# Performance work log

Hardware: AMD Instinct MI355X
Metric: run time of the kernel (lower is better)

The kernel has to match this reference:

```python
import jax, jax.numpy as jnp
import numpy as np

D_MODEL = 1024
NUM_HEADS = 16
DEPTH = D_MODEL // NUM_HEADS
MAX_REL_POS = 128


def setup_inputs() -> dict:
    key = jax.random.key(0)
    ks = jax.random.split(key, 12)
    B, S = 2, 2048
    inp = {
        "q": jax.random.normal(ks[0], (B, S, D_MODEL), jnp.float32),
        "k": jax.random.normal(ks[1], (B, S, D_MODEL), jnp.float32),
        "v": jax.random.normal(ks[2], (B, S, D_MODEL), jnp.float32),
        "mask": jnp.zeros((B, 1, 1, S), jnp.float32),
        "wq": jax.random.normal(ks[3], (D_MODEL, D_MODEL), jnp.float32) * (D_MODEL ** -0.5),
        "bq": jnp.zeros((D_MODEL,), jnp.float32),
        "wk": jax.random.normal(ks[4], (D_MODEL, D_MODEL), jnp.float32) * (D_MODEL ** -0.5),
        "bk": jnp.zeros((D_MODEL,), jnp.float32),
        "wv": jax.random.normal(ks[5], (D_MODEL, D_MODEL), jnp.float32) * (D_MODEL ** -0.5),
        "bv": jnp.zeros((D_MODEL,), jnp.float32),
        "wo": jax.random.normal(ks[6], (D_MODEL, D_MODEL), jnp.float32) * (D_MODEL ** -0.5),
        "bo": jnp.zeros((D_MODEL,), jnp.float32),
        "rel_k_emb": jax.random.normal(ks[7], (2 * MAX_REL_POS + 1, DEPTH), jnp.float32) * 0.02,
        "rel_v_emb": jax.random.normal(ks[8], (2 * MAX_REL_POS + 1, DEPTH), jnp.float32) * 0.02,
    }
    return inp


def _split_heads(x, B):
    # [B, S, d_model] -> [B, H, S, depth]
    S = x.shape[1]
    return x.reshape(B, S, NUM_HEADS, DEPTH).transpose(0, 2, 1, 3)


def reference(q, k, v, mask, wq, bq, wk, bk, wv, bv, wo, bo, rel_k_emb, rel_v_emb):
    B, S, _ = q.shape
    qh = _split_heads(q @ wq + bq, B)  # [B,H,S,d]
    kh = _split_heads(k @ wk + bk, B)
    vh = _split_heads(v @ wv + bv, B)

    # relative position indices [S, S] in [0, 2*MAX_REL_POS]
    ar = jnp.arange(S)
    dist = jnp.clip(ar[None, :] - ar[:, None], -MAX_REL_POS, MAX_REL_POS) + MAX_REL_POS
    rk = rel_k_emb[dist]  # [S, S, depth]
    rv = rel_v_emb[dist]  # [S, S, depth]

    logits = jnp.einsum("bhqd,bhkd->bhqk", qh, kh)
    logits = logits + jnp.einsum("bhqd,qkd->bhqk", qh, rk)
    logits = logits * (1.0 / jnp.sqrt(jnp.float32(DEPTH)))
    logits = logits + mask * -1e9
    attn = jax.nn.softmax(logits, axis=-1)  # [B,H,Sq,Sk]

    out = jnp.einsum("bhqk,bhkd->bhqd", attn, vh)
    out = out + jnp.einsum("bhqk,qkd->bhqd", attn, rv)

    out = out.transpose(0, 2, 1, 3).reshape(B, S, D_MODEL)
    out = out @ wo + bo
    return out, attn
```

## Files before the change

### kernel.cpp

```cpp
#include <hip/hip_runtime.h>
#include <hip/hip_bf16.h>
#include <cstdint>
#include <cstddef>

#define DM   1024
#define NH   16
#define DH   64
#define SEQ  2048
#define BB   2
#define NREL 257
#define BHN  (BB*NH)
#define ROWS (BB*SEQ)

typedef __attribute__((ext_vector_type(8))) short bf16x8;
typedef __attribute__((ext_vector_type(4))) float f32x4;
typedef __attribute__((ext_vector_type(8))) unsigned short us8;

__device__ __forceinline__ unsigned short f2bf(float x){
  union { float f; unsigned u; } v; v.f = x;
  unsigned r = v.u + 0x7fffu + ((v.u >> 16) & 1u);
  return (unsigned short)(r >> 16);
}
__device__ __forceinline__ float b2f(unsigned short h){
  union { unsigned u; float f; } v; v.u = ((unsigned)h) << 16;
  return v.f;
}

__device__ __forceinline__ void gload_lds16(const void* g, void* l){
  __builtin_amdgcn_global_load_lds((const __attribute__((address_space(1))) unsigned int*)g,
                                   (__attribute__((address_space(3))) unsigned int*)l, 16, 0, 0);
}


__global__ void k_split(const float* __restrict__ x, unsigned short* __restrict__ hi,
                        unsigned short* __restrict__ lo, int n){
  int i = blockIdx.x*blockDim.x + threadIdx.x;
  int st = gridDim.x*blockDim.x;
  for (; i < n; i += st){
    float v = x[i];
    unsigned short h = f2bf(v);
    hi[i] = h;
    lo[i] = f2bf(v - b2f(h));
  }
}

__global__ void k_wtrans(const float* __restrict__ W, unsigned short* __restrict__ Thi,
                         unsigned short* __restrict__ Tlo){
  __shared__ float t[64][65];
  int k0 = blockIdx.x*64, n0 = blockIdx.y*64;
  int tid = threadIdx.x;
  for (int u = tid; u < 4096; u += 256){
    int r = u >> 6, c = u & 63;
    t[r][c] = W[(size_t)(k0+r)*DM + n0 + c];
  }
  __syncthreads();
  for (int u = tid; u < 4096; u += 256){
    int r = u >> 6, c = u & 63;
    float v = t[c][r];
    unsigned short h = f2bf(v);
    size_t o = (size_t)(n0+r)*DM + k0 + c;
    Thi[o] = h;
    Tlo[o] = f2bf(v - b2f(h));
  }
}

__global__ void k_embk(const float* __restrict__ e, unsigned short* __restrict__ eb){
  int i = blockIdx.x*256 + threadIdx.x;
  if (i >= 272*64) return;
  int r = i >> 6;
  eb[i] = (r < NREL) ? f2bf(e[i]) : (unsigned short)0;
}

__global__ void k_embt(const float* __restrict__ rv, unsigned short* __restrict__ embT){
  int i = blockIdx.x*256 + threadIdx.x;
  if (i >= 64*256) return;
  int d = i >> 8, j = i & 255;
  embT[i] = (j < 255) ? f2bf(rv[(size_t)(j+1)*DH + d]) : (unsigned short)0;
}

__launch_bounds__(256, 2)
__global__ void k_proj(const unsigned short* __restrict__ Ahi, const unsigned short* __restrict__ Alo,
                       const unsigned short* __restrict__ Bhi, const unsigned short* __restrict__ Blo,
                       const float* __restrict__ bias,
                       unsigned short* __restrict__ Ohi, unsigned short* __restrict__ Olo,
                       int write_lo){
  __shared__ __align__(16) unsigned short sm[4*4096];
  const int tid = threadIdx.x;
  const int w = tid >> 6, lane = tid & 63;
  const int m0 = (blockIdx.x >> 3) * 128;
  const int n0 = (blockIdx.x & 7) * 128;
  const int wr = (w >> 1) * 64, wc = (w & 1) * 64;
  const int fr = lane & 15, fo = (lane >> 4) * 8, fq = (lane >> 4) * 4;

  f32x4 acc[4][4] = {};
  for (int k0 = 0; k0 < DM; k0 += 32){
    const unsigned short* srcs[4] = {
      Ahi + (size_t)m0*DM + k0, Alo + (size_t)m0*DM + k0,
      Bhi + (size_t)n0*DM + k0, Blo + (size_t)n0*DM + k0 };
#pragma unroll
    for (int t = 0; t < 4; ++t)
#pragma unroll
      for (int p = 0; p < 2; ++p){
        int o = p*4096 + tid*16;
        int row = o >> 6, cb = o & 63;
        const char* g = (const char*)(srcs[t] + (size_t)row*DM) + cb;
        char* l = ((char*)sm) + t*8192 + o;
        gload_lds16(g, l);
      }
    __syncthreads();
    bf16x8 a_hi[4], a_lo[4], b_hi[4], b_lo[4];
#pragma unroll
    for (int i = 0; i < 4; ++i){
      int rA = wr + i*16 + fr;
      a_hi[i] = *(const bf16x8*)&sm[0*4096 + rA*32 + fo];
      a_lo[i] = *(const bf16x8*)&sm[1*4096 + rA*32 + fo];
      int rB = wc + i*16 + fr;
      b_hi[i] = *(const bf16x8*)&sm[2*4096 + rB*32 + fo];
      b_lo[i] = *(const bf16x8*)&sm[3*4096 + rB*32 + fo];
    }
#pragma unroll
    for (int i = 0; i < 4; ++i)
#pragma unroll
      for (int j = 0; j < 4; ++j){
        acc[i][j] = __builtin_amdgcn_mfma_f32_16x16x32_bf16(a_hi[i], b_hi[j], acc[i][j], 0,0,0);
        acc[i][j] = __builtin_amdgcn_mfma_f32_16x16x32_bf16(a_hi[i], b_lo[j], acc[i][j], 0,0,0);
        acc[i][j] = __builtin_amdgcn_mfma_f32_16x16x32_bf16(a_lo[i], b_hi[j], acc[i][j], 0,0,0);
      }
    __syncthreads();
  }
#pragma unroll
  for (int i = 0; i < 4; ++i)
#pragma unroll
    for (int j = 0; j < 4; ++j){
      int col = n0 + wc + j*16 + fr;
      float bs = bias[col];
      int h = col >> 6, d = col & 63;
#pragma unroll
      for (int r = 0; r < 4; ++r){
        int row = m0 + wr + i*16 + fq + r;
        int b = row >> 11, s = row & 2047;
        float v = acc[i][j][r] + bs;
        size_t o = ((size_t)(b*NH + h)*SEQ + s)*DH + d;
        unsigned short hh = f2bf(v);
        Ohi[o] = hh;
        if (write_lo) Olo[o] = f2bf(v - b2f(hh));
      }
    }
}

__global__ void k_vtrans(const unsigned short* __restrict__ vh, unsigned short* __restrict__ vt){
  __shared__ __align__(16) unsigned short t[64][72];
  int bh = blockIdx.x >> 5, st = blockIdx.x & 31;
  int s0 = st*64;
  int tid = threadIdx.x;
#pragma unroll
  for (int p = 0; p < 2; ++p){
    int u = tid + p*256;
    int row = u >> 3, ch = u & 7;
    *(us8*)&t[row][ch*8] = *(const us8*)(vh + ((size_t)bh*SEQ + s0 + row)*DH + ch*8);
  }
  __syncthreads();
#pragma unroll
  for (int p = 0; p < 2; ++p){
    int u = tid + p*256;
    int dr = u >> 3, ch = u & 7;
    us8 v;
#pragma unroll
    for (int j = 0; j < 8; ++j) v[j] = t[ch*8+j][dr];
    *(us8*)(vt + ((size_t)bh*DH + dr)*SEQ + s0 + ch*8) = v;
  }
}

__launch_bounds__(256, 2)
__global__ void k_attn(const unsigned short* __restrict__ qhi, const unsigned short* __restrict__ qlo,
                       const unsigned short* __restrict__ khi, const unsigned short* __restrict__ klo,
                       const unsigned short* __restrict__ vt, const unsigned short* __restrict__ embk,
                       const float* __restrict__ mask,
                       unsigned short* __restrict__ Pb, float* __restrict__ Zout,
                       float* __restrict__ ctxu){
  __shared__ unsigned short qrl[64*NREL];
  __shared__ __align__(16) unsigned short Kh[64][72], Kl[64][72], Vt[64][72], Pl[64][72];
  __shared__ float mls[SEQ];

  const int tid = threadIdx.x, w = tid >> 6, lane = tid & 63;
  const int bh = blockIdx.x >> 5, qt = blockIdx.x & 31;
  const int b = bh >> 4;
  const int q0 = qt * 64;
  const int fr = lane & 15, fo = (lane >> 4) * 8, fq = (lane >> 4) * 4;

  for (int i = tid; i < SEQ; i += 256) mls[i] = mask[b*SEQ + i] * (-1e9f);

  bf16x8 q_hi[2], q_lo[2];
  {
    size_t base = ((size_t)bh*SEQ + q0 + w*16 + fr) * DH;
#pragma unroll
    for (int ks = 0; ks < 2; ++ks){
      q_hi[ks] = *(const bf16x8*)(qhi + base + ks*32 + fo);
      q_lo[ks] = *(const bf16x8*)(qlo + base + ks*32 + fo);
    }
  }

#pragma unroll 1
  for (int jt = 0; jt < 17; ++jt){
    f32x4 a = {};
#pragma unroll
    for (int ks = 0; ks < 2; ++ks){
      bf16x8 e = *(const bf16x8*)(embk + ((size_t)(jt*16 + fr))*DH + ks*32 + fo);
      a = __builtin_amdgcn_mfma_f32_16x16x32_bf16(q_hi[ks], e, a, 0,0,0);
    }
    int rr = jt*16 + fr;
#pragma unroll
    for (int r = 0; r < 4; ++r){
      if (rr < NREL) qrl[(w*16 + fq + r)*NREL + rr] = f2bf(a[r]);
    }
  }
  float rcL[4], rcR[4];
#pragma unroll
  for (int r = 0; r < 4; ++r){
    int ql = w*16 + fq + r;
    rcL[r] = b2f(qrl[ql*NREL + 0])   * 0.125f;
    rcR[r] = b2f(qrl[ql*NREL + 256]) * 0.125f;
  }

  const unsigned short* kb_hi = khi + (size_t)bh*SEQ*DH;
  const unsigned short* kb_lo = klo + (size_t)bh*SEQ*DH;
  const unsigned short* vb    = vt  + (size_t)bh*DH*SEQ;

  const int srow = tid >> 3, sch = (tid & 7) * 8;
  us8 rKh[2], rKl[2], rVt[2];
  auto issue = [&](int kt){
#pragma unroll
    for (int p = 0; p < 2; ++p){
      int row = srow + p*32;
      rKh[p] = *(const us8*)(kb_hi + ((size_t)(kt*64 + row))*DH + sch);
      rKl[p] = *(const us8*)(kb_lo + ((size_t)(kt*64 + row))*DH + sch);
      rVt[p] = *(const us8*)(vb + ((size_t)row)*SEQ + kt*64 + sch);
    }
  };
  auto commit = [&](){
#pragma unroll
    for (int p = 0; p < 2; ++p){
      int row = srow + p*32;
      *(us8*)&Kh[row][sch] = rKh[p];
      *(us8*)&Kl[row][sch] = rKl[p];
      *(us8*)&Vt[row][sch] = rVt[p];
    }
  };

  float zpart[4] = {0.f,0.f,0.f,0.f};
  f32x4 ctx[4] = {};

  issue(0); commit();
  __syncthreads();

#pragma unroll 1
  for (int kt = 0; kt < 32; ++kt){
    if (kt < 31) issue(kt + 1);

    const bool leftU  = (kt*64 + 191) <= q0;
    const bool rightU = (kt*64) >= (q0 + 191);

    float pv[4][4];
#pragma unroll
    for (int c = 0; c < 4; ++c){
      f32x4 a = {};
#pragma unroll
      for (int ks = 0; ks < 2; ++ks){
        bf16x8 kf = *(const bf16x8*)&Kh[c*16 + fr][ks*32 + fo];
        bf16x8 lf = *(const bf16x8*)&Kl[c*16 + fr][ks*32 + fo];
        a = __builtin_amdgcn_mfma_f32_16x16x32_bf16(q_hi[ks], kf, a, 0,0,0);
        a = __builtin_amdgcn_mfma_f32_16x16x32_bf16(q_hi[ks], lf, a, 0,0,0);
        a = __builtin_amdgcn_mfma_f32_16x16x32_bf16(q_lo[ks], kf, a, 0,0,0);
      }
      int kg = kt*64 + c*16 + fr;
      float mv = mls[kg];
      if (leftU){
#pragma unroll
        for (int r = 0; r < 4; ++r)
          pv[c][r] = __expf(a[r]*0.125f + rcL[r] + mv);
      } else if (rightU){
#pragma unroll
        for (int r = 0; r < 4; ++r)
          pv[c][r] = __expf(a[r]*0.125f + rcR[r] + mv);
      } else {
#pragma unroll
        for (int r = 0; r < 4; ++r){
          int ql = w*16 + fq + r;
          int qg = q0 + ql;
          int dd = kg - qg; dd = min(max(dd, -128), 128);
          float rel = b2f(qrl[ql*NREL + dd + 128]);
          pv[c][r] = __expf((a[r] + rel)*0.125f + mv);
        }
      }
    }
#pragma unroll
    for (int r = 0; r < 4; ++r)
      zpart[r] += pv[0][r] + pv[1][r] + pv[2][r] + pv[3][r];
#pragma unroll
    for (int c = 0; c < 4; ++c)
#pragma unroll
      for (int r = 0; r < 4; ++r)
        Pl[w*16 + fq + r][c*16 + fr] = f2bf(pv[c][r]);
    {
      int lr = lane >> 2, ch = lane & 3;
      const unsigned short* src = &Pl[w*16 + lr][0];
      size_t gbase = ((size_t)bh*SEQ + q0 + w*16 + lr)*SEQ + kt*64;
      *(us8*)(Pb + gbase + ch*8)     = *(const us8*)(src + ch*8);
      *(us8*)(Pb + gbase + (ch+4)*8) = *(const us8*)(src + (ch+4)*8);
    }
#pragma unroll
    for (int ks = 0; ks < 2; ++ks){
      bf16x8 pf = *(const bf16x8*)&Pl[w*16 + fr][ks*32 + fo];
#pragma unroll
      for (int j = 0; j < 4; ++j){
        bf16x8 vf = *(const bf16x8*)&Vt[j*16 + fr][ks*32 + fo];
        ctx[j] = __builtin_amdgcn_mfma_f32_16x16x32_bf16(pf, vf, ctx[j], 0,0,0);
      }
    }
    if (kt < 31){
      __syncthreads();
      commit();
      __syncthreads();
    }
  }

#pragma unroll
  for (int r = 0; r < 4; ++r){
    float part = zpart[r];
    part += __shfl_xor(part, 1);
    part += __shfl_xor(part, 2);
    part += __shfl_xor(part, 4);
    part += __shfl_xor(part, 8);
    zpart[r] = part;
  }
  if (fr == 0){
#pragma unroll
    for (int r = 0; r < 4; ++r)
      Zout[(size_t)bh*SEQ + q0 + w*16 + fq + r] = zpart[r];
  }
#pragma unroll
  for (int j = 0; j < 4; ++j)
#pragma unroll
    for (int r = 0; r < 4; ++r)
      ctxu[((size_t)bh*SEQ + q0 + w*16 + fq + r)*DH + j*16 + fr] = ctx[j][r];
}

__launch_bounds__(256, 4)
__global__ void k_norm(const unsigned short* __restrict__ Pb, float* __restrict__ attn,
                       const float* __restrict__ Z,
                       const float* __restrict__ ctxu, const unsigned short* __restrict__ embT,
                       const float* __restrict__ rv, unsigned short* __restrict__ ctxb){
  __shared__ __align__(16) unsigned short band[64*256];
  __shared__ float invr[64], Lr[64], Rr[64];
  const int tid = threadIdx.x, w = tid >> 6, lane = tid & 63;
  const int bh = blockIdx.x >> 5, qt = blockIdx.x & 31;
  const int q0 = qt * 64;
  const int fr = lane & 15, fo = (lane >> 4) * 8, fq = (lane >> 4) * 4;

  {
    us8 z = {0,0,0,0,0,0,0,0};
    for (int i = tid; i < 64*256/8; i += 256) ((us8*)band)[i] = z;
  }
  __syncthreads();

#pragma unroll 1
  for (int rr = 0; rr < 16; ++rr){
    int rl = w*16 + rr;
    int q = q0 + rl;
    size_t R = (size_t)bh*SEQ + q;
    float inv = 1.0f / Z[R];
    float la = 0.f, ra = 0.f;
    const us8* prow = (const us8*)(Pb + R*SEQ);
    float4* orow = (float4*)(attn + R*SEQ);
    unsigned short* brow = band + rl*256;
    const int sw = (rl & 7) << 3;
#pragma unroll 1
    for (int c = 0; c < 4; ++c){
      us8 p8 = prow[c*64 + lane];
      float pe[8];
#pragma unroll
      for (int e = 0; e < 8; ++e) pe[e] = b2f(p8[e]);
      float4 o0 = {pe[0]*inv, pe[1]*inv, pe[2]*inv, pe[3]*inv};
      float4 o1 = {pe[4]*inv, pe[5]*inv, pe[6]*inv, pe[7]*inv};
      orow[(c*64 + lane)*2]     = o0;
      orow[(c*64 + lane)*2 + 1] = o1;
      int jlo = c*512 - q + 127;
      if (jlo + 511 < 0){
        la += pe[0]+pe[1]+pe[2]+pe[3]+pe[4]+pe[5]+pe[6]+pe[7];
      } else if (jlo > 254){
        ra += pe[0]+pe[1]+pe[2]+pe[3]+pe[4]+pe[5]+pe[6]+pe[7];
      } else {
        int jb = jlo + lane*8;
#pragma unroll
        for (int e = 0; e < 8; ++e){
          int j = jb + e;
          if (j < 0)        la += pe[e];
          else if (j > 254) ra += pe[e];
          else              brow[j ^ sw] = p8[e];
        }
      }
    }
#pragma unroll
    for (int m = 1; m < 64; m <<= 1){
      la += __shfl_xor(la, m);
      ra += __shfl_xor(ra, m);
    }
    if (lane == 0){ invr[rl] = inv; Lr[rl] = la; Rr[rl] = ra; }
  }
  __syncthreads();

  f32x4 acc[4] = {};
  {
    const int arow = w*16 + fr;
    const int asw = (arow & 7) << 3;
    const unsigned short* bandr = band + arow*256;
#pragma unroll
    for (int kk = 0; kk < 8; ++kk){
      bf16x8 af = *(const bf16x8*)&bandr[(kk*32 + fo) ^ asw];
#pragma unroll
      for (int jt = 0; jt < 4; ++jt){
        bf16x8 bfr = *(const bf16x8*)(embT + (size_t)(jt*16 + fr)*256 + kk*32 + fo);
        acc[jt] = __builtin_amdgcn_mfma_f32_16x16x32_bf16(af, bfr, acc[jt], 0,0,0);
      }
    }
  }

  const int b = bh >> 4, h = bh & 15;
#pragma unroll
  for (int jt = 0; jt < 4; ++jt){
    int d = jt*16 + fr;
    float e0 = rv[d], e256 = rv[(size_t)256*DH + d];
#pragma unroll
    for (int r = 0; r < 4; ++r){
      int rl = w*16 + fq + r;
      int q = q0 + rl;
      float cv = (ctxu[((size_t)bh*SEQ + q)*DH + d] + acc[jt][r] + Lr[rl]*e0 + Rr[rl]*e256) * invr[rl];
      ctxb[((size_t)b*SEQ + q)*DM + h*DH + d] = f2bf(cv);
    }
  }
}

__launch_bounds__(256, 2)
__global__ void k_out(const unsigned short* __restrict__ A, const unsigned short* __restrict__ Bt,
                      const float* __restrict__ bias, float* __restrict__ out){
  __shared__ __align__(16) unsigned short sm[2*4096];
  const int tid = threadIdx.x;
  const int w = tid >> 6, lane = tid & 63;
  const int m0 = (blockIdx.x >> 3) * 128;
  const int n0 = (blockIdx.x & 7) * 128;
  const int wr = (w >> 1) * 64, wc = (w & 1) * 64;
  const int fr = lane & 15, fo = (lane >> 4)*8, fq = (lane >> 4)*4;
  f32x4 acc[4][4] = {};
  for (int k0 = 0; k0 < DM; k0 += 32){
    const unsigned short* srcs[2] = { A + (size_t)m0*DM + k0, Bt + (size_t)n0*DM + k0 };
#pragma unroll
    for (int t = 0; t < 2; ++t)
#pragma unroll
      for (int p = 0; p < 2; ++p){
        int o = p*4096 + tid*16;
        int row = o >> 6, cb = o & 63;
        const char* g = (const char*)(srcs[t] + (size_t)row*DM) + cb;
        char* l = ((char*)sm) + t*8192 + o;
        gload_lds16(g, l);
      }
    __syncthreads();
    bf16x8 af[4], bf[4];
#pragma unroll
    for (int i = 0; i < 4; ++i){
      af[i] = *(const bf16x8*)&sm[0*4096 + (wr + i*16 + fr)*32 + fo];
      bf[i] = *(const bf16x8*)&sm[1*4096 + (wc + i*16 + fr)*32 + fo];
    }
#pragma unroll
    for (int i = 0; i < 4; ++i)
#pragma unroll
      for (int j = 0; j < 4; ++j)
        acc[i][j] = __builtin_amdgcn_mfma_f32_16x16x32_bf16(af[i], bf[j], acc[i][j], 0,0,0);
    __syncthreads();
  }
#pragma unroll
  for (int i = 0; i < 4; ++i)
#pragma unroll
    for (int j = 0; j < 4; ++j){
      int col = n0 + wc + j*16 + fr;
      float bs = bias[col];
#pragma unroll
      for (int r = 0; r < 4; ++r){
        int row = m0 + wr + i*16 + fq + r;
        out[(size_t)row*DM + col] = acc[i][j][r] + bs;
      }
    }
}

extern "C" void kernel_launch(void* const* d_in, const int* in_sizes, int n_in,
                              void* d_out, int out_size, void* d_ws, size_t ws_size,
                              hipStream_t stream){
  const float* q    = (const float*)d_in[0];
  const float* k    = (const float*)d_in[1];
  const float* v    = (const float*)d_in[2];
  const float* mask = (const float*)d_in[3];
  const float* wq   = (const float*)d_in[4];
  const float* bq   = (const float*)d_in[5];
  const float* wk   = (const float*)d_in[6];
  const float* bk   = (const float*)d_in[7];
  const float* wv   = (const float*)d_in[8];
  const float* bv   = (const float*)d_in[9];
  const float* wo   = (const float*)d_in[10];
  const float* bo   = (const float*)d_in[11];
  const float* rk   = (const float*)d_in[12];
  const float* rv   = (const float*)d_in[13];

  float* out  = (float*)d_out;
  float* attn = out + (size_t)ROWS*DM;

  char* p = (char*)d_ws;
  size_t used = 0;
  auto alloc = [&](size_t bytes) -> char* {
    char* r = p;
    size_t a = (bytes + 255) & ~(size_t)255;
    p += a; used += a;
    return r;
  };
  const size_t NE  = (size_t)ROWS*DM;
  unsigned short* q_hi = (unsigned short*)alloc(NE*2);
  unsigned short* q_lo = (unsigned short*)alloc(NE*2);
  unsigned short* k_hi = (unsigned short*)alloc(NE*2);
  unsigned short* k_lo = (unsigned short*)alloc(NE*2);
  unsigned short* v_hi = (unsigned short*)alloc(NE*2);
  unsigned short* v_lo = (unsigned short*)alloc(NE*2);
  unsigned short* wqt_hi = (unsigned short*)alloc((size_t)DM*DM*2);
  unsigned short* wqt_lo = (unsigned short*)alloc((size_t)DM*DM*2);
  unsigned short* wkt_hi = (unsigned short*)alloc((size_t)DM*DM*2);
  unsigned short* wkt_lo = (unsigned short*)alloc((size_t)DM*DM*2);
  unsigned short* wvt_hi = (unsigned short*)alloc((size_t)DM*DM*2);
  unsigned short* wvt_lo = (unsigned short*)alloc((size_t)DM*DM*2);
  unsigned short* wot_hi = (unsigned short*)alloc((size_t)DM*DM*2);
  unsigned short* wot_lo = (unsigned short*)alloc((size_t)DM*DM*2);
  unsigned short* qh_hi = (unsigned short*)alloc(NE*2);
  unsigned short* qh_lo = (unsigned short*)alloc(NE*2);
  unsigned short* kh_hi = (unsigned short*)alloc(NE*2);
  unsigned short* kh_lo = (unsigned short*)alloc(NE*2);
  unsigned short* vh    = (unsigned short*)alloc(NE*2);
  unsigned short* vht   = (unsigned short*)alloc(NE*2);
  unsigned short* embk  = (unsigned short*)alloc((size_t)272*64*2);
  unsigned short* embT  = (unsigned short*)alloc((size_t)64*256*2);
  float* Zb   = (float*)alloc((size_t)BHN*SEQ*4);
  float* ctxu = (float*)alloc((size_t)BHN*SEQ*DH*4);
  unsigned short* ctxb = (unsigned short*)alloc(NE*2);
  unsigned short* Pb   = (unsigned short*)alloc((size_t)BHN*SEQ*SEQ*2);
  if (used > ws_size) return;

  int n = (int)NE;
  k_split<<<2048, 256, 0, stream>>>(q, q_hi, q_lo, n);
  k_split<<<2048, 256, 0, stream>>>(k, k_hi, k_lo, n);
  k_split<<<2048, 256, 0, stream>>>(v, v_hi, v_lo, n);
  dim3 tg(16,16);
  k_wtrans<<<tg, 256, 0, stream>>>(wq, wqt_hi, wqt_lo);
  k_wtrans<<<tg, 256, 0, stream>>>(wk, wkt_hi, wkt_lo);
  k_wtrans<<<tg, 256, 0, stream>>>(wv, wvt_hi, wvt_lo);
  k_wtrans<<<tg, 256, 0, stream>>>(wo, wot_hi, wot_lo);
  k_embk<<<(272*64+255)/256, 256, 0, stream>>>(rk, embk);
  k_embt<<<64, 256, 0, stream>>>(rv, embT);

  k_proj<<<256, 256, 0, stream>>>(q_hi, q_lo, wqt_hi, wqt_lo, bq, qh_hi, qh_lo, 1);
  k_proj<<<256, 256, 0, stream>>>(k_hi, k_lo, wkt_hi, wkt_lo, bk, kh_hi, kh_lo, 1);
  k_proj<<<256, 256, 0, stream>>>(v_hi, v_lo, wvt_hi, wvt_lo, bv, vh, vh, 0);
  k_vtrans<<<1024, 256, 0, stream>>>(vh, vht);

  k_attn<<<1024, 256, 0, stream>>>(qh_hi, qh_lo, kh_hi, kh_lo, vht, embk, mask, Pb, Zb, ctxu);
  k_norm<<<1024, 256, 0, stream>>>(Pb, attn, Zb, ctxu, embT, rv, ctxb);
  k_out<<<256, 256, 0, stream>>>(ctxb, wot_hi, bo, out);
}
```

Measured before the change: 625.8 us.

## Drop split-bf16 compensation and use plain bf16 for projections and QK logits

Removes the hi/lo bf16 split emulation of fp32 throughout: inputs and weights are cast once to single bf16, projections use one MFMA per tile instead of three, and the QK^T logits in attention use a single bf16 product. This cuts MFMA work, LDS traffic and workspace memory traffic for the split buffers, and the input cast is vectorized to float4. The trade is reduced accuracy in the logits and projections, which may push results toward the tolerance limit. It also clamps the embedding load indices so padded entries no longer read out of bounds.

```diff
diff --git a/kernel.cpp b/kernel.cpp
--- a/kernel.cpp
+++ b/kernel.cpp
@@ -15,6 +15,7 @@
 typedef __attribute__((ext_vector_type(8))) short bf16x8;
 typedef __attribute__((ext_vector_type(4))) float f32x4;
 typedef __attribute__((ext_vector_type(8))) unsigned short us8;
+typedef __attribute__((ext_vector_type(4))) unsigned short us4;
 
 __device__ __forceinline__ unsigned short f2bf(float x){
   union { float f; unsigned u; } v; v.f = x;
@@ -32,20 +33,17 @@
 }
 
 
-__global__ void k_split(const float* __restrict__ x, unsigned short* __restrict__ hi,
-                        unsigned short* __restrict__ lo, int n){
+__global__ void k_cast(const float* __restrict__ x, unsigned short* __restrict__ o, int n4){
   int i = blockIdx.x*blockDim.x + threadIdx.x;
   int st = gridDim.x*blockDim.x;
-  for (; i < n; i += st){
-    float v = x[i];
-    unsigned short h = f2bf(v);
-    hi[i] = h;
-    lo[i] = f2bf(v - b2f(h));
-  }
-}
-
-__global__ void k_wtrans(const float* __restrict__ W, unsigned short* __restrict__ Thi,
-                         unsigned short* __restrict__ Tlo){
+  for (; i < n4; i += st){
+    float4 f = ((const float4*)x)[i];
+    us4 v = { f2bf(f.x), f2bf(f.y), f2bf(f.z), f2bf(f.w) };
+    *(us4*)(o + (size_t)i*4) = v;
+  }
+}
+
+__global__ void k_wtrans(const float* __restrict__ W, unsigned short* __restrict__ T){
   __shared__ float t[64][65];
   int k0 = blockIdx.x*64, n0 = blockIdx.y*64;
   int tid = threadIdx.x;
@@ -56,11 +54,7 @@
   __syncthreads();
   for (int u = tid; u < 4096; u += 256){
     int r = u >> 6, c = u & 63;
-    float v = t[c][r];
-    unsigned short h = f2bf(v);
-    size_t o = (size_t)(n0+r)*DM + k0 + c;
-    Thi[o] = h;
-    Tlo[o] = f2bf(v - b2f(h));
+    T[(size_t)(n0+r)*DM + k0 + c] = f2bf(t[c][r]);
   }
 }
 
@@ -68,37 +62,33 @@
   int i = blockIdx.x*256 + threadIdx.x;
   if (i >= 272*64) return;
   int r = i >> 6;
-  eb[i] = (r < NREL) ? f2bf(e[i]) : (unsigned short)0;
+  float v = e[min(i, NREL*64 - 1)];
+  eb[i] = (r < NREL) ? f2bf(v) : (unsigned short)0;
 }
 
 __global__ void k_embt(const float* __restrict__ rv, unsigned short* __restrict__ embT){
   int i = blockIdx.x*256 + threadIdx.x;
   if (i >= 64*256) return;
   int d = i >> 8, j = i & 255;
-  embT[i] = (j < 255) ? f2bf(rv[(size_t)(j+1)*DH + d]) : (unsigned short)0;
+  float v = rv[(size_t)min(j+1, 256)*DH + d];
+  embT[i] = (j < 255) ? f2bf(v) : (unsigned short)0;
 }
 
 __launch_bounds__(256, 2)
-__global__ void k_proj(const unsigned short* __restrict__ Ahi, const unsigned short* __restrict__ Alo,
-                       const unsigned short* __restrict__ Bhi, const unsigned short* __restrict__ Blo,
-                       const float* __restrict__ bias,
-                       unsigned short* __restrict__ Ohi, unsigned short* __restrict__ Olo,
-                       int write_lo){
-  __shared__ __align__(16) unsigned short sm[4*4096];
+__global__ void k_proj(const unsigned short* __restrict__ A, const unsigned short* __restrict__ Bt,
+                       const float* __restrict__ bias, unsigned short* __restrict__ O){
+  __shared__ __align__(16) unsigned short sm[2*4096];
   const int tid = threadIdx.x;
   const int w = tid >> 6, lane = tid & 63;
   const int m0 = (blockIdx.x >> 3) * 128;
   const int n0 = (blockIdx.x & 7) * 128;
   const int wr = (w >> 1) * 64, wc = (w & 1) * 64;
-  const int fr = lane & 15, fo = (lane >> 4) * 8, fq = (lane >> 4) * 4;
-
+  const int fr = lane & 15, fo = (lane >> 4)*8, fq = (lane >> 4)*4;
   f32x4 acc[4][4] = {};
   for (int k0 = 0; k0 < DM; k0 += 32){
-    const unsigned short* srcs[4] = {
-      Ahi + (size_t)m0*DM + k0, Alo + (size_t)m0*DM + k0,
-      Bhi + (size_t)n0*DM + k0, Blo + (size_t)n0*DM + k0 };
-#pragma unroll
-    for (int t = 0; t < 4; ++t)
+    const unsigned short* srcs[2] = { A + (size_t)m0*DM + k0, Bt + (size_t)n0*DM + k0 };
+#pragma unroll
+    for (int t = 0; t < 2; ++t)
 #pragma unroll
       for (int p = 0; p < 2; ++p){
         int o = p*4096 + tid*16;
@@ -108,24 +98,17 @@
         gload_lds16(g, l);
       }
     __syncthreads();
-    bf16x8 a_hi[4], a_lo[4], b_hi[4], b_lo[4];
+    bf16x8 af[4], bf[4];
 #pragma unroll
     for (int i = 0; i < 4; ++i){
-      int rA = wr + i*16 + fr;
-      a_hi[i] = *(const bf16x8*)&sm[0*4096 + rA*32 + fo];
-      a_lo[i] = *(const bf16x8*)&sm[1*4096 + rA*32 + fo];
-      int rB = wc + i*16 + fr;
-      b_hi[i] = *(const bf16x8*)&sm[2*4096 + rB*32 + fo];
-      b_lo[i] = *(const bf16x8*)&sm[3*4096 + rB*32 + fo];
+      af[i] = *(const bf16x8*)&sm[0*4096 + (wr + i*16 + fr)*32 + fo];
+      bf[i] = *(const bf16x8*)&sm[1*4096 + (wc + i*16 + fr)*32 + fo];
     }
 #pragma unroll
     for (int i = 0; i < 4; ++i)
 #pragma unroll
-      for (int j = 0; j < 4; ++j){
-        acc[i][j] = __builtin_amdgcn_mfma_f32_16x16x32_bf16(a_hi[i], b_hi[j], acc[i][j], 0,0,0);
-        acc[i][j] = __builtin_amdgcn_mfma_f32_16x16x32_bf16(a_hi[i], b_lo[j], acc[i][j], 0,0,0);
-        acc[i][j] = __builtin_amdgcn_mfma_f32_16x16x32_bf16(a_lo[i], b_hi[j], acc[i][j], 0,0,0);
-      }
+      for (int j = 0; j < 4; ++j)
+        acc[i][j] = __builtin_amdgcn_mfma_f32_16x16x32_bf16(af[i], bf[j], acc[i][j], 0,0,0);
     __syncthreads();
   }
 #pragma unroll
@@ -139,11 +122,7 @@
       for (int r = 0; r < 4; ++r){
         int row = m0 + wr + i*16 + fq + r;
         int b = row >> 11, s = row & 2047;
-        float v = acc[i][j][r] + bs;
-        size_t o = ((size_t)(b*NH + h)*SEQ + s)*DH + d;
-        unsigned short hh = f2bf(v);
-        Ohi[o] = hh;
-        if (write_lo) Olo[o] = f2bf(v - b2f(hh));
+        O[((size_t)(b*NH + h)*SEQ + s)*DH + d] = f2bf(acc[i][j][r] + bs);
       }
     }
 }
@@ -172,14 +151,13 @@
 }
 
 __launch_bounds__(256, 2)
-__global__ void k_attn(const unsigned short* __restrict__ qhi, const unsigned short* __restrict__ qlo,
-                       const unsigned short* __restrict__ khi, const unsigned short* __restrict__ klo,
+__global__ void k_attn(const unsigned short* __restrict__ qh, const unsigned short* __restrict__ kh,
                        const unsigned short* __restrict__ vt, const unsigned short* __restrict__ embk,
                        const float* __restrict__ mask,
                        unsigned short* __restrict__ Pb, float* __restrict__ Zout,
                        float* __restrict__ ctxu){
   __shared__ unsigned short qrl[64*NREL];
-  __shared__ __align__(16) unsigned short Kh[64][72], Kl[64][72], Vt[64][72], Pl[64][72];
+  __shared__ __align__(16) unsigned short Kh[64][72], Vt[64][72], Pl[64][72];
   __shared__ float mls[SEQ];
 
   const int tid = threadIdx.x, w = tid >> 6, lane = tid & 63;
@@ -190,14 +168,12 @@
 
   for (int i = tid; i < SEQ; i += 256) mls[i] = mask[b*SEQ + i] * (-1e9f);
 
-  bf16x8 q_hi[2], q_lo[2];
+  bf16x8 q_hi[2];
   {
     size_t base = ((size_t)bh*SEQ + q0 + w*16 + fr) * DH;
 #pragma unroll
-    for (int ks = 0; ks < 2; ++ks){
-      q_hi[ks] = *(const bf16x8*)(qhi + base + ks*32 + fo);
-      q_lo[ks] = *(const bf16x8*)(qlo + base + ks*32 + fo);
-    }
+    for (int ks = 0; ks < 2; ++ks)
+      q_hi[ks] = *(const bf16x8*)(qh + base + ks*32 + fo);
   }
 
 #pragma unroll 1
@@ -222,18 +198,16 @@
     rcR[r] = b2f(qrl[ql*NREL + 256]) * 0.125f;
   }
 
-  const unsigned short* kb_hi = khi + (size_t)bh*SEQ*DH;
-  const unsigned short* kb_lo = klo + (size_t)bh*SEQ*DH;
-  const unsigned short* vb    = vt  + (size_t)bh*DH*SEQ;
+  const unsigned short* kb = kh + (size_t)bh*SEQ*DH;
+  const unsigned short* vb = vt + (size_t)bh*DH*SEQ;
 
   const int srow = tid >> 3, sch = (tid & 7) * 8;
-  us8 rKh[2], rKl[2], rVt[2];
+  us8 rKh[2], rVt[2];
   auto issue = [&](int kt){
 #pragma unroll
     for (int p = 0; p < 2; ++p){
       int row = srow + p*32;
-      rKh[p] = *(const us8*)(kb_hi + ((size_t)(kt*64 + row))*DH + sch);
-      rKl[p] = *(const us8*)(kb_lo + ((size_t)(kt*64 + row))*DH + sch);
+      rKh[p] = *(const us8*)(kb + ((size_t)(kt*64 + row))*DH + sch);
       rVt[p] = *(const us8*)(vb + ((size_t)row)*SEQ + kt*64 + sch);
     }
   };
@@ -242,7 +216,6 @@
     for (int p = 0; p < 2; ++p){
       int row = srow + p*32;
       *(us8*)&Kh[row][sch] = rKh[p];
-      *(us8*)&Kl[row][sch] = rKl[p];
       *(us8*)&Vt[row][sch] = rVt[p];
     }
   };
@@ -267,10 +240,7 @@
 #pragma unroll
       for (int ks = 0; ks < 2; ++ks){
         bf16x8 kf = *(const bf16x8*)&Kh[c*16 + fr][ks*32 + fo];
-        bf16x8 lf = *(const bf16x8*)&Kl[c*16 + fr][ks*32 + fo];
         a = __builtin_amdgcn_mfma_f32_16x16x32_bf16(q_hi[ks], kf, a, 0,0,0);
-        a = __builtin_amdgcn_mfma_f32_16x16x32_bf16(q_hi[ks], lf, a, 0,0,0);
-        a = __builtin_amdgcn_mfma_f32_16x16x32_bf16(q_lo[ks], kf, a, 0,0,0);
       }
       int kg = kt*64 + c*16 + fr;
       float mv = mls[kg];
@@ -521,52 +491,43 @@
     return r;
   };
   const size_t NE  = (size_t)ROWS*DM;
-  unsigned short* q_hi = (unsigned short*)alloc(NE*2);
-  unsigned short* q_lo = (unsigned short*)alloc(NE*2);
-  unsigned short* k_hi = (unsigned short*)alloc(NE*2);
-  unsigned short* k_lo = (unsigned short*)alloc(NE*2);
-  unsigned short* v_hi = (unsigned short*)alloc(NE*2);
-  unsigned short* v_lo = (unsigned short*)alloc(NE*2);
-  unsigned short* wqt_hi = (unsigned short*)alloc((size_t)DM*DM*2);
-  unsigned short* wqt_lo = (unsigned short*)alloc((size_t)DM*DM*2);
-  unsigned short* wkt_hi = (unsigned short*)alloc((size_t)DM*DM*2);
-  unsigned short* wkt_lo = (unsigned short*)alloc((size_t)DM*DM*2);
-  unsigned short* wvt_hi = (unsigned short*)alloc((size_t)DM*DM*2);
-  unsigned short* wvt_lo = (unsigned short*)alloc((size_t)DM*DM*2);
-  unsigned short* wot_hi = (unsigned short*)alloc((size_t)DM*DM*2);
-  unsigned short* wot_lo = (unsigned short*)alloc((size_t)DM*DM*2);
-  unsigned short* qh_hi = (unsigned short*)alloc(NE*2);
-  unsigned short* qh_lo = (unsigned short*)alloc(NE*2);
-  unsigned short* kh_hi = (unsigned short*)alloc(NE*2);
-  unsigned short* kh_lo = (unsigned short*)alloc(NE*2);
-  unsigned short* vh    = (unsigned short*)alloc(NE*2);
-  unsigned short* vht   = (unsigned short*)alloc(NE*2);
-  unsigned short* embk  = (unsigned short*)alloc((size_t)272*64*2);
-  unsigned short* embT  = (unsigned short*)alloc((size_t)64*256*2);
+  unsigned short* qb   = (unsigned short*)alloc(NE*2);
+  unsigned short* kbf  = (unsigned short*)alloc(NE*2);
+  unsigned short* vbf  = (unsigned short*)alloc(NE*2);
+  unsigned short* wqt  = (unsigned short*)alloc((size_t)DM*DM*2);
+  unsigned short* wkt  = (unsigned short*)alloc((size_t)DM*DM*2);
+  unsigned short* wvt  = (unsigned short*)alloc((size_t)DM*DM*2);
+  unsigned short* wot  = (unsigned short*)alloc((size_t)DM*DM*2);
+  unsigned short* qh   = (unsigned short*)alloc(NE*2);
+  unsigned short* kh   = (unsigned short*)alloc(NE*2);
+  unsigned short* vh   = (unsigned short*)alloc(NE*2);
+  unsigned short* vht  = (unsigned short*)alloc(NE*2);
+  unsigned short* embk = (unsigned short*)alloc((size_t)272*64*2);
+  unsigned short* embT = (unsigned short*)alloc((size_t)64*256*2);
   float* Zb   = (float*)alloc((size_t)BHN*SEQ*4);
   float* ctxu = (float*)alloc((size_t)BHN*SEQ*DH*4);
   unsigned short* ctxb = (unsigned short*)alloc(NE*2);
   unsigned short* Pb   = (unsigned short*)alloc((size_t)BHN*SEQ*SEQ*2);
   if (used > ws_size) return;
 
-  int n = (int)NE;
-  k_split<<<2048, 256, 0, stream>>>(q, q_hi, q_lo, n);
-  k_split<<<2048, 256, 0, stream>>>(k, k_hi, k_lo, n);
-  k_split<<<2048, 256, 0, stream>>>(v, v_hi, v_lo, n);
+  const int N4 = (int)(NE/4);
+  k_cast<<<2048, 256, 0, stream>>>(q, qb, N4);
+  k_cast<<<2048, 256, 0, stream>>>(k, kbf, N4);
+  k_cast<<<2048, 256, 0, stream>>>(v, vbf, N4);
   dim3 tg(16,16);
-  k_wtrans<<<tg, 256, 0, stream>>>(wq, wqt_hi, wqt_lo);
-  k_wtrans<<<tg, 256, 0, stream>>>(wk, wkt_hi, wkt_lo);
-  k_wtrans<<<tg, 256, 0, stream>>>(wv, wvt_hi, wvt_lo);
-  k_wtrans<<<tg, 256, 0, stream>>>(wo, wot_hi, wot_lo);
+  k_wtrans<<<tg, 256, 0, stream>>>(wq, wqt);
+  k_wtrans<<<tg, 256, 0, stream>>>(wk, wkt);
+  k_wtrans<<<tg, 256, 0, stream>>>(wv, wvt);
+  k_wtrans<<<tg, 256, 0, stream>>>(wo, wot);
   k_embk<<<(272*64+255)/256, 256, 0, stream>>>(rk, embk);
   k_embt<<<64, 256, 0, stream>>>(rv, embT);
 
-  k_proj<<<256, 256, 0, stream>>>(q_hi, q_lo, wqt_hi, wqt_lo, bq, qh_hi, qh_lo, 1);
-  k_proj<<<256, 256, 0, stream>>>(k_hi, k_lo, wkt_hi, wkt_lo, bk, kh_hi, kh_lo, 1);
-  k_proj<<<256, 256, 0, stream>>>(v_hi, v_lo, wvt_hi, wvt_lo, bv, vh, vh, 0);
+  k_proj<<<256, 256, 0, stream>>>(qb,  wqt, bq, qh);
+  k_proj<<<256, 256, 0, stream>>>(kbf, wkt, bk, kh);
+  k_proj<<<256, 256, 0, stream>>>(vbf, wvt, bv, vh);
   k_vtrans<<<1024, 256, 0, stream>>>(vh, vht);
 
-  k_attn<<<1024, 256, 0, stream>>>(qh_hi, qh_lo, kh_hi, kh_lo, vht, embk, mask, Pb, Zb, ctxu);
+  k_attn<<<1024, 256, 0, stream>>>(qh, kh, vht, embk, mask, Pb, Zb, ctxu);
   k_norm<<<1024, 256, 0, stream>>>(Pb, attn, Zb, ctxu, embT, rv, ctxb);
-  k_out<<<256, 256, 0, stream>>>(ctxb, wot_hi, bo, out);
-}
+  k_out<<<256, 256, 0, stream>>>(ctxb, wot, bo, out);
+}
```

Result: faster. 511.5 us, median of 3 (-18.3%).
